# Kernel tuning notes

Measured on AMD Instinct MI355X. Metric: run time of the kernel, lower is better.

The kernel has to match this reference:

```python
import jax, jax.numpy as jnp
import numpy as np

N, E = 50000, 800000
F_IN, H, C = 128, 4, 32
NEG_SLOPE = 0.2

def setup_inputs() -> dict:
    key = jax.random.key(0)
    k1, k2, k3, k4, k5, k6 = jax.random.split(key, 6)
    x = jax.random.normal(k1, (N, F_IN), dtype=jnp.float32)
    edge_index = jax.random.randint(k2, (2, E), 0, N, dtype=jnp.int64)
    # GATConv params: lin weight [F_IN, H*C], att_src/att_dst [H, C], bias [H*C]
    W = jax.random.normal(k3, (F_IN, H * C), dtype=jnp.float32) * (1.0 / np.sqrt(F_IN))
    att_src = jax.random.normal(k4, (H, C), dtype=jnp.float32) * (1.0 / np.sqrt(C))
    att_dst = jax.random.normal(k5, (H, C), dtype=jnp.float32) * (1.0 / np.sqrt(C))
    bias = jax.random.normal(k6, (H * C,), dtype=jnp.float32) * 0.01
    return {"x": x, "edge_index": edge_index, "W": W, "att_src": att_src, "att_dst": att_dst, "bias": bias}

def reference(x, edge_index, W, att_src, att_dst, bias):
    # Linear transform: [N, H, C]
    h = (x @ W).reshape(N, H, C)
    # Per-node attention logits: [N, H]
    a_src = jnp.einsum('nhc,hc->nh', h, att_src)
    a_dst = jnp.einsum('nhc,hc->nh', h, att_dst)
    # PyG GATConv adds self-loops by default
    loop = jnp.arange(N, dtype=edge_index.dtype)
    src = jnp.concatenate([edge_index[0], loop])  # message source j
    dst = jnp.concatenate([edge_index[1], loop])  # message target i
    # Edge logits + LeakyReLU: [E+N, H]
    e = jax.nn.leaky_relu(a_src[src] + a_dst[dst], NEG_SLOPE)
    # Segment softmax over incoming edges per target node
    m = jax.ops.segment_max(e, dst, num_segments=N)  # [N, H]
    e_exp = jnp.exp(e - m[dst])
    denom = jax.ops.segment_sum(e_exp, dst, num_segments=N)  # [N, H]
    att = e_exp / denom[dst]  # [E+N, H]
    # Scatter-add weighted messages: [N, H, C]
    out = jax.ops.segment_sum(h[src] * att[:, :, None], dst, num_segments=N)
    return out.reshape(N, H * C) + bias
```

## Files before the change

kernel.cpp:

```cpp
#include <hip/hip_runtime.h>
#include <cstdint>

#define NNODES 50000
#define NEDGES 800000
#define NEG 0.2f
#define NBKT 196
#define BCAP 5120
#define GEMM_BLOCKS 782

typedef __attribute__((ext_vector_type(8))) short short8;
typedef __attribute__((ext_vector_type(4))) float f32x4;

#define AS_STRIDE 136
#define CS_STRIDE 132

__device__ __forceinline__ float leaky(float v) { return v > 0.f ? v : NEG * v; }

__device__ __forceinline__ unsigned short f2bf(float f) {
    unsigned int u = __float_as_uint(f);
    u += 0x7fff + ((u >> 16) & 1);
    return (unsigned short)(u >> 16);
}

template <int NW>
__device__ __forceinline__ int block_excl_scan(int v, int t) {
    __shared__ int wsum[NW];
    const int lane = t & 63, wv = t >> 6;
    int x = v;
    #pragma unroll
    for (int m = 1; m < 64; m <<= 1) {
        int u = __shfl_up(x, m);
        if (lane >= m) x += u;
    }
    if (lane == 63) wsum[wv] = x;
    __syncthreads();
    if (t == 0) {
        int run = 0;
        #pragma unroll
        for (int i = 0; i < NW; ++i) { int tmp = wsum[i]; wsum[i] = run; run += tmp; }
    }
    __syncthreads();
    return x - v + wsum[wv];
}

__global__ __launch_bounds__(256) void wt_k(const float* __restrict__ W,
                                            const float* __restrict__ att_src,
                                            const float* __restrict__ att_dst,
                                            unsigned short* __restrict__ wt,
                                            uint4* __restrict__ battf,
                                            int* __restrict__ bcnt) {
    const int t = threadIdx.x;
    if (blockIdx.x < 16) {
        int i = blockIdx.x * 256 + t;
        int k = i >> 5, n4 = (i & 31) * 4;
        float4 wv = ((const float4*)W)[i];
        wt[(n4 + 0) * 128 + k] = f2bf(wv.x);
        wt[(n4 + 1) * 128 + k] = f2bf(wv.y);
        wt[(n4 + 2) * 128 + k] = f2bf(wv.z);
        wt[(n4 + 3) * 128 + k] = f2bf(wv.w);
        return;
    }
    __shared__ float wsd[2][128][4];
    if (t < NBKT) bcnt[t] = 0;
    const int k = t & 127, which = t >> 7;
    const float* av = which ? att_dst : att_src;
    #pragma unroll
    for (int h = 0; h < 4; ++h) {
        float s = 0.f;
        #pragma unroll
        for (int c4 = 0; c4 < 8; ++c4) {
            float4 wv = ((const float4*)(W + k * 128 + h * 32))[c4];
            float4 a  = ((const float4*)(av + h * 32))[c4];
            s += wv.x * a.x + wv.y * a.y + wv.z * a.z + wv.w * a.w;
        }
        wsd[which][k][h] = s;
    }
    __syncthreads();
    const int s = t >> 6, lane = t & 63;
    const int quad = lane >> 4, m16 = lane & 15;
    unsigned short fr[8];
    #pragma unroll
    for (int j = 0; j < 8; ++j) {
        int kk = s * 32 + quad * 8 + j;
        float v = 0.f;
        if (m16 < 4)      v = wsd[0][kk][m16];
        else if (m16 < 8) v = wsd[1][kk][m16 - 4];
        fr[j] = f2bf(v);
    }
    battf[s * 64 + lane] = make_uint4(
        ((unsigned)fr[1] << 16) | fr[0], ((unsigned)fr[3] << 16) | fr[2],
        ((unsigned)fr[5] << 16) | fr[4], ((unsigned)fr[7] << 16) | fr[6]);
}

__global__ __launch_bounds__(256) void fused_k(const float* __restrict__ x,
                                               const unsigned short* __restrict__ wt,
                                               const uint4* __restrict__ battf,
                                               unsigned short* __restrict__ hb,
                                               float* __restrict__ a_src,
                                               float* __restrict__ a_dst,
                                               const int* __restrict__ ei,
                                               int* __restrict__ bcnt,
                                               unsigned int* __restrict__ bktdata) {
    __shared__ __align__(16) char smem[52224];
    const int tid = threadIdx.x;

    if (blockIdx.x < GEMM_BLOCKS) {
        unsigned short* As = (unsigned short*)smem;
        unsigned short* Bs = (unsigned short*)(smem + 17408);
        float*          Cs = (float*)smem;
        const int rbase = blockIdx.x * 64;

        #pragma unroll
        for (int i = 0; i < 8; ++i) {
            int f = tid + i * 256;
            int r = f >> 5, c4 = (f & 31) * 4;
            float4 xv = make_float4(0.f, 0.f, 0.f, 0.f);
            if (rbase + r < NNODES) xv = ((const float4*)x)[(size_t)(rbase + r) * 32 + (f & 31)];
            unsigned int p0 = ((unsigned int)f2bf(xv.y) << 16) | f2bf(xv.x);
            unsigned int p1 = ((unsigned int)f2bf(xv.w) << 16) | f2bf(xv.z);
            *(uint2*)(As + r * AS_STRIDE + c4) = make_uint2(p0, p1);
        }
        #pragma unroll
        for (int i = 0; i < 8; ++i) {
            int c = tid + i * 256;
            int n = c >> 4, k8 = (c & 15) * 8;
            uint4 wv = ((const uint4*)wt)[c];
            *(uint4*)(Bs + n * AS_STRIDE + k8) = wv;
        }
        __syncthreads();

        const int lane = tid & 63, w = tid >> 6;
        const int quad = lane >> 4, m16 = lane & 15;

        short8 af[4];
        #pragma unroll
        for (int s = 0; s < 4; ++s)
            af[s] = *(const short8*)(As + (w * 16 + m16) * AS_STRIDE + s * 32 + quad * 8);

        f32x4 acc[8];
        #pragma unroll
        for (int t = 0; t < 8; ++t) acc[t] = (f32x4){0.f, 0.f, 0.f, 0.f};

        #pragma unroll
        for (int t = 0; t < 8; ++t) {
            #pragma unroll
            for (int s = 0; s < 4; ++s) {
                short8 bf = *(const short8*)(Bs + (t * 16 + m16) * AS_STRIDE + s * 32 + quad * 8);
                acc[t] = __builtin_amdgcn_mfma_f32_16x16x32_bf16(af[s], bf, acc[t], 0, 0, 0);
            }
        }

        f32x4 accL = (f32x4){0.f, 0.f, 0.f, 0.f};
        #pragma unroll
        for (int s = 0; s < 4; ++s) {
            uint4 bw = battf[s * 64 + lane];
            accL = __builtin_amdgcn_mfma_f32_16x16x32_bf16(af[s], *(short8*)&bw, accL, 0, 0, 0);
        }
        __syncthreads();

        #pragma unroll
        for (int t = 0; t < 8; ++t)
            #pragma unroll
            for (int r = 0; r < 4; ++r)
                Cs[(w * 16 + quad * 4 + r) * CS_STRIDE + t * 16 + m16] = acc[t][r];
        __syncthreads();

        const int cp = lane;
        #pragma unroll
        for (int r = 0; r < 16; ++r) {
            int row = w * 16 + r;
            int row_g = rbase + row;
            float2 cv = *(const float2*)(Cs + row * CS_STRIDE + 2 * cp);
            ushort2 hs;
            hs.x = f2bf(cv.x); hs.y = f2bf(cv.y);
            if (row_g < NNODES) ((ushort2*)(hb + (size_t)row_g * 128))[cp] = hs;
        }
        #pragma unroll
        for (int r = 0; r < 4; ++r) {
            int row_g = rbase + w * 16 + quad * 4 + r;
            if (row_g < NNODES) {
                if (m16 < 4)      a_src[row_g * 4 + m16]       = accL[r];
                else if (m16 < 8) a_dst[row_g * 4 + (m16 - 4)] = accL[r];
            }
        }
    } else {
        int* lhist = (int*)smem;
        int* lofs  = lhist + NBKT;
        int* lcur  = lofs + NBKT;
        int* gbase = lcur + NBKT;
        unsigned int* staged = (unsigned int*)(gbase + NBKT);
        const int b = blockIdx.x - GEMM_BLOCKS, t = tid;
        for (int i = t; i < NBKT; i += 256) lhist[i] = 0;
        __syncthreads();
        unsigned int pk[16];
        int bk[16];
        const int e0 = b * 4096;
        #pragma unroll
        for (int i = 0; i < 16; ++i) {
            int e = e0 + i * 256 + t;
            if (e < NEDGES) {
                int s = ei[e], d = ei[NEDGES + e];
                bk[i] = d >> 8;
                pk[i] = ((unsigned)bk[i] << 24) | ((unsigned)(d & 255) << 16) | (unsigned)s;
                atomicAdd(&lhist[bk[i]], 1);
            } else bk[i] = -1;
        }
        __syncthreads();
        int v = (t < NBKT) ? lhist[t] : 0;
        int excl = block_excl_scan<4>(v, t);
        if (t < NBKT) { lofs[t] = excl; lcur[t] = excl; }
        __syncthreads();
        if (t < NBKT) gbase[t] = (v > 0) ? atomicAdd(&bcnt[t], v) : 0;
        #pragma unroll
        for (int i = 0; i < 16; ++i) {
            if (bk[i] >= 0) {
                int pos = atomicAdd(&lcur[bk[i]], 1);
                staged[pos] = pk[i];
            }
        }
        __syncthreads();
        const int total = lofs[NBKT - 1] + lhist[NBKT - 1];
        for (int i = t; i < total; i += 256) {
            unsigned int ent = staged[i];
            int bb = ent >> 24;
            int pos = gbase[bb] + (i - lofs[bb]);
            bktdata[(size_t)bb * BCAP + pos] = ent & 0x00FFFFFFu;
        }
    }
}

__global__ __launch_bounds__(512) void sort_k(const int* __restrict__ bcnt,
                                              const unsigned int* __restrict__ bktdata,
                                              int* __restrict__ off,
                                              int* __restrict__ csr) {
    __shared__ unsigned int staged[BCAP];
    __shared__ int lcnt[256];
    __shared__ int lcur[256];
    __shared__ int sbase, scnt;
    const int b = blockIdx.x, t = threadIdx.x;
    int bv = (t < NBKT) ? bcnt[t] : 0;
    int bexcl = block_excl_scan<8>(bv, t);
    if (t == b) { sbase = bexcl; scnt = bv; }
    if (t < 256) lcnt[t] = 0;
    __syncthreads();
    const int cnt = scnt, base = sbase;
    for (int i = t; i < cnt; i += 512) staged[i] = bktdata[(size_t)b * BCAP + i];
    __syncthreads();
    for (int i = t; i < cnt; i += 512) atomicAdd(&lcnt[(staged[i] >> 16) & 0xFF], 1);
    __syncthreads();
    int v = (t < 256) ? lcnt[t] : 0;
    int excl = block_excl_scan<8>(v, t);
    if (t < 256) {
        lcur[t] = excl;
        const int node = b * 256 + t;
        if (node <= NNODES) off[node] = base + excl;
    }
    __syncthreads();
    for (int i = t; i < cnt; i += 512) {
        unsigned int ent = staged[i];
        int pos = atomicAdd(&lcur[(ent >> 16) & 0xFF], 1);
        csr[base + pos] = (int)(ent & 0xFFFFu);
    }
}

__global__ __launch_bounds__(256) void gather_k(const int* __restrict__ off,
                                                const int* __restrict__ csr,
                                                const unsigned short* __restrict__ hb,
                                                const float* __restrict__ a_src,
                                                const float* __restrict__ a_dst,
                                                const float* __restrict__ bias,
                                                float* __restrict__ out) {
    const int wid = threadIdx.x >> 6, lane = threadIdx.x & 63;
    const int n = blockIdx.x * 4 + wid;
    if (n >= NNODES) return;
    const int g = lane >> 4;
    const int q = lane & 15;
    const int head_c = q >> 2;

    const float adn = a_dst[n * 4 + head_c];
    const float wsc = __expf(leaky(a_src[n * 4 + head_c] + adn));

    float acc[8];
    #pragma unroll
    for (int k = 0; k < 8; ++k) acc[k] = 0.f;
    float den = 0.f;

    if (g == 0) {
        uint4 hv = ((const uint4*)(hb + (size_t)n * 128))[q];
        acc[0] = wsc * __uint_as_float(hv.x << 16);
        acc[1] = wsc * __uint_as_float(hv.x & 0xffff0000u);
        acc[2] = wsc * __uint_as_float(hv.y << 16);
        acc[3] = wsc * __uint_as_float(hv.y & 0xffff0000u);
        acc[4] = wsc * __uint_as_float(hv.z << 16);
        acc[5] = wsc * __uint_as_float(hv.z & 0xffff0000u);
        acc[6] = wsc * __uint_as_float(hv.w << 16);
        acc[7] = wsc * __uint_as_float(hv.w & 0xffff0000u);
    }

    const int beg = off[n], end = off[n + 1];
    for (int base = beg; base < end; base += 16) {
        const int m = end - base < 16 ? end - base : 16;
        int sj[4];
        float as4[4];
        uint4 hv4[4];
        #pragma unroll
        for (int jj = 0; jj < 4; ++jj) {
            int e = base + jj * 4 + g;
            if (e > end - 1) e = end - 1;
            sj[jj] = csr[e];
        }
        #pragma unroll
        for (int jj = 0; jj < 4; ++jj) as4[jj] = a_src[sj[jj] * 4 + head_c];
        #pragma unroll
        for (int jj = 0; jj < 4; ++jj)
            hv4[jj] = ((const uint4*)(hb + (size_t)sj[jj] * 128))[q];
        #pragma unroll
        for (int jj = 0; jj < 4; ++jj) {
            const int j = jj * 4 + g;
            float w = __expf(leaky(as4[jj] + adn));
            w = (j < m) ? w : 0.f;
            den += w;
            acc[0] += w * __uint_as_float(hv4[jj].x << 16);
            acc[1] += w * __uint_as_float(hv4[jj].x & 0xffff0000u);
            acc[2] += w * __uint_as_float(hv4[jj].y << 16);
            acc[3] += w * __uint_as_float(hv4[jj].y & 0xffff0000u);
            acc[4] += w * __uint_as_float(hv4[jj].z << 16);
            acc[5] += w * __uint_as_float(hv4[jj].z & 0xffff0000u);
            acc[6] += w * __uint_as_float(hv4[jj].w << 16);
            acc[7] += w * __uint_as_float(hv4[jj].w & 0xffff0000u);
        }
    }
    #pragma unroll
    for (int k = 0; k < 8; ++k) {
        acc[k] += __shfl_xor(acc[k], 16);
        acc[k] += __shfl_xor(acc[k], 32);
    }
    den += __shfl_xor(den, 16);
    den += __shfl_xor(den, 32);
    if (g == 0) {
        const float inv = __frcp_rn(den + wsc);
        float4 b0 = ((const float4*)bias)[2 * q];
        float4 b1 = ((const float4*)bias)[2 * q + 1];
        float4* orow = (float4*)(out + (size_t)n * 128);
        orow[2 * q]     = make_float4(acc[0] * inv + b0.x, acc[1] * inv + b0.y,
                                      acc[2] * inv + b0.z, acc[3] * inv + b0.w);
        orow[2 * q + 1] = make_float4(acc[4] * inv + b1.x, acc[5] * inv + b1.y,
                                      acc[6] * inv + b1.z, acc[7] * inv + b1.w);
    }
}

extern "C" void kernel_launch(void* const* d_in, const int* in_sizes, int n_in,
                              void* d_out, int out_size, void* d_ws, size_t ws_size,
                              hipStream_t stream) {
    const float* x     = (const float*)d_in[0];
    const int*   ei    = (const int*)d_in[1];
    const float* W     = (const float*)d_in[2];
    const float* att_s = (const float*)d_in[3];
    const float* att_d = (const float*)d_in[4];
    const float* bias  = (const float*)d_in[5];
    float*       out   = (float*)d_out;
    char*        ws    = (char*)d_ws;

    unsigned short* hb = (unsigned short*)(ws);
    float* a_src  = (float*)(ws + 12800000);
    float* a_dst  = (float*)(ws + 13600000);
    int*   off    = (int*)  (ws + 14400000);
    int*   csr    = (int*)  (ws + 14600768);
    unsigned int* bktdata = (unsigned int*)(ws + 17800768);
    int*   bcnt   = (int*)  (ws + 21814848);
    unsigned short* wt = (unsigned short*)(ws + 21815632);
    uint4* battf  = (uint4*)(ws + 21848400);

    wt_k    <<<17, 256, 0, stream>>>(W, att_s, att_d, wt, battf, bcnt);
    fused_k <<<GEMM_BLOCKS + NBKT, 256, 0, stream>>>(x, wt, battf, hb,
                                                     a_src, a_dst, ei, bcnt, bktdata);
    sort_k  <<<NBKT, 512, 0, stream>>>(bcnt, bktdata, off, csr);
    gather_k<<<12500, 256, 0, stream>>>(off, csr, hb, a_src, a_dst, bias, out);
}
```

Measured before the change: 148.6 us.

## Regroup stages: bucket edges in prep kernel, overlap sort with GEMM

Edge bucketing moves out of the GEMM kernel into the weight-prep kernel. The per-bucket counting sort, formerly its own 512-thread kernel, now runs in the first blocks of the GEMM kernel with 256 threads. This removes one kernel launch and lets the sort overlap with the GEMM. The bucket counters are now cleared with a memset, which is an extra stream operation, and the sort blocks have half as many threads per bucket.

```diff
diff --git a/kernel.cpp b/kernel.cpp
--- a/kernel.cpp
+++ b/kernel.cpp
@@ -43,72 +43,146 @@
     return x - v + wsum[wv];
 }
 
-__global__ __launch_bounds__(256) void wt_k(const float* __restrict__ W,
-                                            const float* __restrict__ att_src,
-                                            const float* __restrict__ att_dst,
-                                            unsigned short* __restrict__ wt,
-                                            uint4* __restrict__ battf,
-                                            int* __restrict__ bcnt) {
+__global__ __launch_bounds__(256) void prep_k(const float* __restrict__ W,
+                                              const float* __restrict__ att_src,
+                                              const float* __restrict__ att_dst,
+                                              unsigned short* __restrict__ wt,
+                                              uint4* __restrict__ battf,
+                                              const int* __restrict__ ei,
+                                              int* __restrict__ bcnt,
+                                              unsigned int* __restrict__ bktdata) {
+    __shared__ __align__(16) char smem[19712];
     const int t = threadIdx.x;
-    if (blockIdx.x < 16) {
-        int i = blockIdx.x * 256 + t;
+
+    if (blockIdx.x < NBKT) {
+        int* lhist = (int*)smem;
+        int* lofs  = lhist + NBKT;
+        int* lcur  = lofs + NBKT;
+        int* gbase = lcur + NBKT;
+        unsigned int* staged = (unsigned int*)(gbase + NBKT);
+        const int b = blockIdx.x;
+        for (int i = t; i < NBKT; i += 256) lhist[i] = 0;
+        __syncthreads();
+        unsigned int pk[16];
+        int bk[16];
+        const int e0 = b * 4096;
+        #pragma unroll
+        for (int i = 0; i < 16; ++i) {
+            int e = e0 + i * 256 + t;
+            if (e < NEDGES) {
+                int s = ei[e], d = ei[NEDGES + e];
+                bk[i] = d >> 8;
+                pk[i] = ((unsigned)bk[i] << 24) | ((unsigned)(d & 255) << 16) | (unsigned)s;
+                atomicAdd(&lhist[bk[i]], 1);
+            } else bk[i] = -1;
+        }
+        __syncthreads();
+        int v = (t < NBKT) ? lhist[t] : 0;
+        int excl = block_excl_scan<4>(v, t);
+        if (t < NBKT) { lofs[t] = excl; lcur[t] = excl; }
+        __syncthreads();
+        if (t < NBKT) gbase[t] = (v > 0) ? atomicAdd(&bcnt[t], v) : 0;
+        #pragma unroll
+        for (int i = 0; i < 16; ++i) {
+            if (bk[i] >= 0) {
+                int pos = atomicAdd(&lcur[bk[i]], 1);
+                staged[pos] = pk[i];
+            }
+        }
+        __syncthreads();
+        const int total = lofs[NBKT - 1] + lhist[NBKT - 1];
+        for (int i = t; i < total; i += 256) {
+            unsigned int ent = staged[i];
+            int bb = ent >> 24;
+            int pos = gbase[bb] + (i - lofs[bb]);
+            bktdata[(size_t)bb * BCAP + pos] = ent & 0x00FFFFFFu;
+        }
+    } else if (blockIdx.x < NBKT + 16) {
+        int i = (blockIdx.x - NBKT) * 256 + t;
         int k = i >> 5, n4 = (i & 31) * 4;
         float4 wv = ((const float4*)W)[i];
         wt[(n4 + 0) * 128 + k] = f2bf(wv.x);
         wt[(n4 + 1) * 128 + k] = f2bf(wv.y);
         wt[(n4 + 2) * 128 + k] = f2bf(wv.z);
         wt[(n4 + 3) * 128 + k] = f2bf(wv.w);
-        return;
-    }
-    __shared__ float wsd[2][128][4];
-    if (t < NBKT) bcnt[t] = 0;
-    const int k = t & 127, which = t >> 7;
-    const float* av = which ? att_dst : att_src;
-    #pragma unroll
-    for (int h = 0; h < 4; ++h) {
-        float s = 0.f;
-        #pragma unroll
-        for (int c4 = 0; c4 < 8; ++c4) {
-            float4 wv = ((const float4*)(W + k * 128 + h * 32))[c4];
-            float4 a  = ((const float4*)(av + h * 32))[c4];
-            s += wv.x * a.x + wv.y * a.y + wv.z * a.z + wv.w * a.w;
-        }
-        wsd[which][k][h] = s;
-    }
-    __syncthreads();
-    const int s = t >> 6, lane = t & 63;
-    const int quad = lane >> 4, m16 = lane & 15;
-    unsigned short fr[8];
-    #pragma unroll
-    for (int j = 0; j < 8; ++j) {
-        int kk = s * 32 + quad * 8 + j;
-        float v = 0.f;
-        if (m16 < 4)      v = wsd[0][kk][m16];
-        else if (m16 < 8) v = wsd[1][kk][m16 - 4];
-        fr[j] = f2bf(v);
-    }
-    battf[s * 64 + lane] = make_uint4(
-        ((unsigned)fr[1] << 16) | fr[0], ((unsigned)fr[3] << 16) | fr[2],
-        ((unsigned)fr[5] << 16) | fr[4], ((unsigned)fr[7] << 16) | fr[6]);
-}
-
-__global__ __launch_bounds__(256) void fused_k(const float* __restrict__ x,
-                                               const unsigned short* __restrict__ wt,
-                                               const uint4* __restrict__ battf,
-                                               unsigned short* __restrict__ hb,
-                                               float* __restrict__ a_src,
-                                               float* __restrict__ a_dst,
-                                               const int* __restrict__ ei,
-                                               int* __restrict__ bcnt,
-                                               unsigned int* __restrict__ bktdata) {
+    } else {
+        float* wsd = (float*)smem;
+        const int k = t & 127, which = t >> 7;
+        const float* av = which ? att_dst : att_src;
+        #pragma unroll
+        for (int h = 0; h < 4; ++h) {
+            float s = 0.f;
+            #pragma unroll
+            for (int c4 = 0; c4 < 8; ++c4) {
+                float4 wv = ((const float4*)(W + k * 128 + h * 32))[c4];
+                float4 a  = ((const float4*)(av + h * 32))[c4];
+                s += wv.x * a.x + wv.y * a.y + wv.z * a.z + wv.w * a.w;
+            }
+            wsd[(which * 128 + k) * 4 + h] = s;
+        }
+        __syncthreads();
+        const int s = t >> 6, lane = t & 63;
+        const int quad = lane >> 4, m16 = lane & 15;
+        unsigned short fr[8];
+        #pragma unroll
+        for (int j = 0; j < 8; ++j) {
+            int kk = s * 32 + quad * 8 + j;
+            float v = 0.f;
+            if (m16 < 4)      v = wsd[(0 * 128 + kk) * 4 + m16];
+            else if (m16 < 8) v = wsd[(1 * 128 + kk) * 4 + (m16 - 4)];
+            fr[j] = f2bf(v);
+        }
+        battf[s * 64 + lane] = make_uint4(
+            ((unsigned)fr[1] << 16) | fr[0], ((unsigned)fr[3] << 16) | fr[2],
+            ((unsigned)fr[5] << 16) | fr[4], ((unsigned)fr[7] << 16) | fr[6]);
+    }
+}
+
+__global__ __launch_bounds__(256) void main_k(const float* __restrict__ x,
+                                              const unsigned short* __restrict__ wt,
+                                              const uint4* __restrict__ battf,
+                                              unsigned short* __restrict__ hb,
+                                              float* __restrict__ a_src,
+                                              float* __restrict__ a_dst,
+                                              const int* __restrict__ bcnt,
+                                              const unsigned int* __restrict__ bktdata,
+                                              int* __restrict__ off,
+                                              int* __restrict__ csr) {
     __shared__ __align__(16) char smem[52224];
     const int tid = threadIdx.x;
 
-    if (blockIdx.x < GEMM_BLOCKS) {
+    if (blockIdx.x < NBKT) {
+        unsigned int* staged = (unsigned int*)smem;
+        int* lcnt = (int*)(smem + 20480);
+        int* lcur = (int*)(smem + 21504);
+        __shared__ int sbase, scnt;
+        const int b = blockIdx.x, t = tid;
+        int bv = (t < NBKT) ? bcnt[t] : 0;
+        int bexcl = block_excl_scan<4>(bv, t);
+        if (t == b) { sbase = bexcl; scnt = bv; }
+        lcnt[t] = 0;
+        __syncthreads();
+        const int cnt = scnt, base = sbase;
+        for (int i = t; i < cnt; i += 256) staged[i] = bktdata[(size_t)b * BCAP + i];
+        __syncthreads();
+        for (int i = t; i < cnt; i += 256) atomicAdd(&lcnt[(staged[i] >> 16) & 0xFF], 1);
+        __syncthreads();
+        int v = lcnt[t];
+        int excl = block_excl_scan<4>(v, t);
+        lcur[t] = excl;
+        const int node = b * 256 + t;
+        if (node <= NNODES) off[node] = base + excl;
+        __syncthreads();
+        for (int i = t; i < cnt; i += 256) {
+            unsigned int ent = staged[i];
+            int pos = atomicAdd(&lcur[(ent >> 16) & 0xFF], 1);
+            csr[base + pos] = (int)(ent & 0xFFFFu);
+        }
+    } else {
         unsigned short* As = (unsigned short*)smem;
         unsigned short* Bs = (unsigned short*)(smem + 17408);
         float*          Cs = (float*)smem;
-        const int rbase = blockIdx.x * 64;
+        const int rbase = (blockIdx.x - NBKT) * 64;
 
         #pragma unroll
         for (int i = 0; i < 8; ++i) {
@@ -183,83 +257,6 @@
                 else if (m16 < 8) a_dst[row_g * 4 + (m16 - 4)] = accL[r];
             }
         }
-    } else {
-        int* lhist = (int*)smem;
-        int* lofs  = lhist + NBKT;
-        int* lcur  = lofs + NBKT;
-        int* gbase = lcur + NBKT;
-        unsigned int* staged = (unsigned int*)(gbase + NBKT);
-        const int b = blockIdx.x - GEMM_BLOCKS, t = tid;
-        for (int i = t; i < NBKT; i += 256) lhist[i] = 0;
-        __syncthreads();
-        unsigned int pk[16];
-        int bk[16];
-        const int e0 = b * 4096;
-        #pragma unroll
-        for (int i = 0; i < 16; ++i) {
-            int e = e0 + i * 256 + t;
-            if (e < NEDGES) {
-                int s = ei[e], d = ei[NEDGES + e];
-                bk[i] = d >> 8;
-                pk[i] = ((unsigned)bk[i] << 24) | ((unsigned)(d & 255) << 16) | (unsigned)s;
-                atomicAdd(&lhist[bk[i]], 1);
-            } else bk[i] = -1;
-        }
-        __syncthreads();
-        int v = (t < NBKT) ? lhist[t] : 0;
-        int excl = block_excl_scan<4>(v, t);
-        if (t < NBKT) { lofs[t] = excl; lcur[t] = excl; }
-        __syncthreads();
-        if (t < NBKT) gbase[t] = (v > 0) ? atomicAdd(&bcnt[t], v) : 0;
-        #pragma unroll
-        for (int i = 0; i < 16; ++i) {
-            if (bk[i] >= 0) {
-                int pos = atomicAdd(&lcur[bk[i]], 1);
-                staged[pos] = pk[i];
-            }
-        }
-        __syncthreads();
-        const int total = lofs[NBKT - 1] + lhist[NBKT - 1];
-        for (int i = t; i < total; i += 256) {
-            unsigned int ent = staged[i];
-            int bb = ent >> 24;
-            int pos = gbase[bb] + (i - lofs[bb]);
-            bktdata[(size_t)bb * BCAP + pos] = ent & 0x00FFFFFFu;
-        }
-    }
-}
-
-__global__ __launch_bounds__(512) void sort_k(const int* __restrict__ bcnt,
-                                              const unsigned int* __restrict__ bktdata,
-                                              int* __restrict__ off,
-                                              int* __restrict__ csr) {
-    __shared__ unsigned int staged[BCAP];
-    __shared__ int lcnt[256];
-    __shared__ int lcur[256];
-    __shared__ int sbase, scnt;
-    const int b = blockIdx.x, t = threadIdx.x;
-    int bv = (t < NBKT) ? bcnt[t] : 0;
-    int bexcl = block_excl_scan<8>(bv, t);
-    if (t == b) { sbase = bexcl; scnt = bv; }
-    if (t < 256) lcnt[t] = 0;
-    __syncthreads();
-    const int cnt = scnt, base = sbase;
-    for (int i = t; i < cnt; i += 512) staged[i] = bktdata[(size_t)b * BCAP + i];
-    __syncthreads();
-    for (int i = t; i < cnt; i += 512) atomicAdd(&lcnt[(staged[i] >> 16) & 0xFF], 1);
-    __syncthreads();
-    int v = (t < 256) ? lcnt[t] : 0;
-    int excl = block_excl_scan<8>(v, t);
-    if (t < 256) {
-        lcur[t] = excl;
-        const int node = b * 256 + t;
-        if (node <= NNODES) off[node] = base + excl;
-    }
-    __syncthreads();
-    for (int i = t; i < cnt; i += 512) {
-        unsigned int ent = staged[i];
-        int pos = atomicAdd(&lcur[(ent >> 16) & 0xFF], 1);
-        csr[base + pos] = (int)(ent & 0xFFFFu);
     }
 }
 
@@ -371,9 +368,11 @@
     unsigned short* wt = (unsigned short*)(ws + 21815632);
     uint4* battf  = (uint4*)(ws + 21848400);
 
-    wt_k    <<<17, 256, 0, stream>>>(W, att_s, att_d, wt, battf, bcnt);
-    fused_k <<<GEMM_BLOCKS + NBKT, 256, 0, stream>>>(x, wt, battf, hb,
-                                                     a_src, a_dst, ei, bcnt, bktdata);
-    sort_k  <<<NBKT, 512, 0, stream>>>(bcnt, bktdata, off, csr);
+    hipMemsetAsync(bcnt, 0, NBKT * sizeof(int), stream);
+    prep_k  <<<NBKT + 17, 256, 0, stream>>>(W, att_s, att_d, wt, battf,
+                                            ei, bcnt, bktdata);
+    main_k  <<<NBKT + GEMM_BLOCKS, 256, 0, stream>>>(x, wt, battf, hb,
+                                                     a_src, a_dst, bcnt, bktdata,
+                                                     off, csr);
     gather_k<<<12500, 256, 0, stream>>>(off, csr, hb, a_src, a_dst, bias, out);
 }
```

Measured after the change: 144.7 us. 1.03x faster.
